# Optimization experiments

Measured on AMD Instinct MI355X. Metric: run time of the kernel, lower is better.

Reference implementation:

```python
import jax, jax.numpy as jnp
import numpy as np

B, S, D, H = 2, 2048, 1024, 16
HD = D // H  # head_dim = 64


def setup_inputs() -> dict:
    key = jax.random.key(0)
    ks = jax.random.split(key, 9)
    sc = 1.0 / np.sqrt(D)
    return {
        "X": jax.random.normal(ks[0], (B, S, D), jnp.float32),
        "Wq": jax.random.normal(ks[1], (D, D), jnp.float32) * sc,
        "bq": jnp.zeros((D,), jnp.float32),
        "Wk": jax.random.normal(ks[2], (D, D), jnp.float32) * sc,
        "bk": jnp.zeros((D,), jnp.float32),
        "Wv": jax.random.normal(ks[3], (D, D), jnp.float32) * sc,
        "bv": jnp.zeros((D,), jnp.float32),
        "Wo": jax.random.normal(ks[4], (D, D), jnp.float32) * sc,
        "bo": jnp.zeros((D,), jnp.float32),
    }


def reference(X, Wq, bq, Wk, bk, Wv, bv, Wo, bo):
    b, s, d = X.shape
    q = (X @ Wq + bq).reshape(b, s, H, HD).transpose(0, 2, 1, 3)  # [B,H,S,HD]
    k = (X @ Wk + bk).reshape(b, s, H, HD).transpose(0, 2, 1, 3)
    v = (X @ Wv + bv).reshape(b, s, H, HD).transpose(0, 2, 1, 3)
    score = jnp.einsum("bhqd,bhkd->bhqk", q, k) / jnp.sqrt(jnp.float32(HD))
    causal = jnp.tril(jnp.ones((s, s), bool))  # [S,S]
    score = jnp.where(causal[None, None], score, -jnp.inf)
    attn = jax.nn.softmax(score, axis=-1)
    out = jnp.einsum("bhqk,bhkd->bhqd", attn, v)  # [B,H,S,HD]
    out = out.transpose(0, 2, 1, 3).reshape(b, s, d)
    return out @ Wo + bo
```

## Files before the change

kernel.cpp:

```cpp
#include <hip/hip_runtime.h>
#include <hip/hip_bf16.h>
#include <math.h>

#define B_SZ 2
#define S_SZ 2048
#define D_SZ 1024
#define H_SZ 16
#define HD_SZ 64
constexpr int M_ROWS = B_SZ * S_SZ;

typedef __bf16 bf16x8 __attribute__((ext_vector_type(8)));
typedef __bf16 bf16x4 __attribute__((ext_vector_type(4)));
typedef float f32x4 __attribute__((ext_vector_type(4)));

#define GLOAD_LDS16(gsrc, ldst)                                              \
  __builtin_amdgcn_global_load_lds(                                          \
      (const __attribute__((address_space(1))) void*)(gsrc),                 \
      (__attribute__((address_space(3))) void*)(ldst), 16, 0, 0)

__global__ __launch_bounds__(256) void cvt_bf16(const float* __restrict__ in,
                                                __bf16* __restrict__ out,
                                                int n8) {
  const int i = blockIdx.x * 256 + threadIdx.x;
  if (i >= n8) return;
  const float4 a = *reinterpret_cast<const float4*>(&in[i * 8]);
  const float4 b = *reinterpret_cast<const float4*>(&in[i * 8 + 4]);
  bf16x8 o;
  o[0] = (__bf16)a.x; o[1] = (__bf16)a.y; o[2] = (__bf16)a.z; o[3] = (__bf16)a.w;
  o[4] = (__bf16)b.x; o[5] = (__bf16)b.y; o[6] = (__bf16)b.z; o[7] = (__bf16)b.w;
  *reinterpret_cast<bf16x8*>(&out[i * 8]) = o;
}

__global__ __launch_bounds__(256) void cvt_w_t_all(const float* __restrict__ W0,
                                                   const float* __restrict__ W1,
                                                   const float* __restrict__ W2,
                                                   const float* __restrict__ W3,
                                                   __bf16* __restrict__ Wt) {
  __shared__ float Ts[32][33];
  const int z = blockIdx.z;
  const float* W = z == 0 ? W0 : (z == 1 ? W1 : (z == 2 ? W2 : W3));
  __bf16* out = Wt + (size_t)z * 1024 * 1024;
  const int k0 = blockIdx.x * 32, n0 = blockIdx.y * 32;
  const int tr = threadIdx.x >> 3;
  const int tc = (threadIdx.x & 7) * 4;
  const float4 v = *reinterpret_cast<const float4*>(&W[(size_t)(k0 + tr) * 1024 + n0 + tc]);
  Ts[tr][tc + 0] = v.x;
  Ts[tr][tc + 1] = v.y;
  Ts[tr][tc + 2] = v.z;
  Ts[tr][tc + 3] = v.w;
  __syncthreads();
  bf16x4 o;
#pragma unroll
  for (int j = 0; j < 4; ++j) o[j] = (__bf16)Ts[tc + j][tr];
  *reinterpret_cast<bf16x4*>(&out[(size_t)(n0 + tr) * 1024 + k0 + tc]) = o;
}

__global__ __launch_bounds__(256) void transpose_v(const __bf16* __restrict__ V,
                                                   __bf16* __restrict__ Vt) {
  constexpr int TST = 66;
  __shared__ __bf16 T[64 * TST];
  const int bh = blockIdx.y;
  const int s0 = blockIdx.x * 64;
  const size_t base = (size_t)bh * S_SZ * HD_SZ;
  const int tid = threadIdx.x;
  for (int i = tid; i < 512; i += 256) {
    const int r = i >> 3, c = (i & 7) * 8;
    *reinterpret_cast<bf16x8*>(&T[r * TST + c]) =
        *reinterpret_cast<const bf16x8*>(&V[base + (size_t)(s0 + r) * 64 + c]);
  }
  __syncthreads();
  const size_t obase = (size_t)bh * HD_SZ * S_SZ;
  for (int i = tid; i < 512; i += 256) {
    const int d = i >> 3, c = (i & 7) * 8;
    bf16x8 o;
#pragma unroll
    for (int j = 0; j < 8; ++j) o[j] = T[(c + j) * TST + d];
    *reinterpret_cast<bf16x8*>(&Vt[obase + (size_t)d * S_SZ + s0 + c]) = o;
  }
}

template <int MODE, int BN>
__global__ __launch_bounds__(256) void gemm_mfma(
    const __bf16* __restrict__ Ab, const __bf16* __restrict__ Bt,
    const float* __restrict__ bias0, const float* __restrict__ bias1,
    const float* __restrict__ bias2, float* __restrict__ C0,
    __bf16* __restrict__ Q0, __bf16* __restrict__ K0, __bf16* __restrict__ V0,
    int M, int N, int K) {
  constexpr int NJ = BN / 32;
  __shared__ __bf16 As[2][128 * 32];
  __shared__ __bf16 Bs[2][BN * 32];
  __shared__ __bf16 Ep[(MODE == 1) ? 32 * 132 : 4];

  const int tid = threadIdx.x;
  const int lane = tid & 63;
  const int w = tid >> 6;
  const int lr = lane & 15, lg = lane >> 4;
  const int wr = w >> 1, wc = w & 1;
  const int bm = blockIdx.x * 128;
  const int bn = blockIdx.y * BN;

  const int r0 = tid >> 2, c0 = (tid & 3) * 8;
  const int r1 = (tid + 256) >> 2, c1 = ((tid + 256) & 3) * 8;
  const __bf16* aS0 = &Ab[(size_t)(bm + r0) * K + c0];
  const __bf16* aS1 = &Ab[(size_t)(bm + r1) * K + c1];
  const __bf16* bS0 = &Bt[(size_t)(bn + r0) * K + c0];
  const __bf16* bS1 = &Bt[(size_t)(bn + r1) * K + c1];

  f32x4 acc[4][NJ] = {};

  auto STAGE = [&](int buf) {
    GLOAD_LDS16(aS0, &As[buf][w * 512]);
    GLOAD_LDS16(aS1, &As[buf][2048 + w * 512]);
    GLOAD_LDS16(bS0, &Bs[buf][w * 512]);
    if constexpr (BN == 128) GLOAD_LDS16(bS1, &Bs[buf][2048 + w * 512]);
    aS0 += 32; aS1 += 32; bS0 += 32;
    if constexpr (BN == 128) bS1 += 32;
  };

  STAGE(0);
  asm volatile("s_waitcnt vmcnt(0)" ::: "memory");
  __builtin_amdgcn_s_barrier();
  __builtin_amdgcn_sched_barrier(0);
  int cur = 0;

  for (int k0 = 0; k0 < K; k0 += 32) {
    const bool has_next = (k0 + 32 < K);
    if (has_next) STAGE(cur ^ 1);
    if (k0) {
      if (has_next) {
        if constexpr (BN == 128)
          asm volatile("s_waitcnt vmcnt(4)" ::: "memory");
        else
          asm volatile("s_waitcnt vmcnt(3)" ::: "memory");
      } else {
        asm volatile("s_waitcnt vmcnt(0)" ::: "memory");
      }
      __builtin_amdgcn_s_barrier();
      __builtin_amdgcn_sched_barrier(0);
    }

    bf16x8 af[4], bfr[NJ];
#pragma unroll
    for (int i = 0; i < 4; ++i)
      af[i] = *reinterpret_cast<const bf16x8*>(&As[cur][(wr * 64 + i * 16 + lr) * 32 + lg * 8]);
#pragma unroll
    for (int j = 0; j < NJ; ++j)
      bfr[j] = *reinterpret_cast<const bf16x8*>(&Bs[cur][(wc * (BN / 2) + j * 16 + lr) * 32 + lg * 8]);
    __builtin_amdgcn_s_setprio(1);
#pragma unroll
    for (int i = 0; i < 4; ++i)
#pragma unroll
      for (int j = 0; j < NJ; ++j)
        acc[i][j] = __builtin_amdgcn_mfma_f32_16x16x32_bf16(af[i], bfr[j], acc[i][j], 0, 0, 0);
    __builtin_amdgcn_s_setprio(0);
    __builtin_amdgcn_sched_barrier(0);
    __builtin_amdgcn_s_barrier();
    cur ^= 1;
  }

  if (MODE == 0) {
#pragma unroll
    for (int j = 0; j < NJ; ++j) {
      const int n = bn + wc * (BN / 2) + j * 16 + lr;
      const float bs = bias0[n];
#pragma unroll
      for (int i = 0; i < 4; ++i) {
        const int mrow = bm + wr * 64 + i * 16 + lg * 4;
#pragma unroll
        for (int r = 0; r < 4; ++r)
          C0[(size_t)(mrow + r) * N + n] = acc[i][j][r] + bs;
      }
    }
  } else {
    const int which = bn >> 10;
    __bf16* dst = which == 0 ? Q0 : (which == 1 ? K0 : V0);
    const float* bp = which == 0 ? bias0 : (which == 1 ? bias1 : bias2);
    const float scale = which == 0 ? 0.18033688011112042f : 1.0f;
    float bias4[4];
#pragma unroll
    for (int j = 0; j < 4; ++j)
      bias4[j] = bp[(bn & 1023) + wc * 64 + j * 16 + lr];

#pragma unroll
    for (int i = 0; i < 4; ++i) {
      __syncthreads();
#pragma unroll
      for (int j = 0; j < 4; ++j) {
        const int colw = wc * 64 + j * 16 + lr;
#pragma unroll
        for (int r = 0; r < 4; ++r)
          Ep[(wr * 16 + lg * 4 + r) * 132 + colw] =
              (__bf16)((acc[i][j][r] + bias4[j]) * scale);
      }
      __syncthreads();
#pragma unroll
      for (int u = 0; u < 2; ++u) {
        const int c = tid + u * 256;
        const int er = c >> 4;
        const int off = (c & 15) * 8;
        const int m = bm + (er >> 4) * 64 + i * 16 + (er & 15);
        const int nn = (bn & 1023) + off;
        const int hh = nn >> 6, hd = nn & 63;
        const int bb = m >> 11, ss = m & (S_SZ - 1);
        *reinterpret_cast<bf16x8*>(
            &dst[(((size_t)(bb * H_SZ + hh)) * S_SZ + ss) * HD_SZ + hd]) =
            *reinterpret_cast<const bf16x8*>(&Ep[er * 132 + off]);
      }
    }
  }
}

__global__ __launch_bounds__(256) void attn_mfma(const __bf16* __restrict__ Q,
                                                 const __bf16* __restrict__ Kg,
                                                 const __bf16* __restrict__ Vtg,
                                                 __bf16* __restrict__ Aout) {
  constexpr int PST = 76;
  __shared__ __bf16 Ks[2][64 * 64];
  __shared__ __bf16 Vts[2][64 * 64];
  __shared__ __bf16 Ps[4][16 * PST];

  const int tid = threadIdx.x;
  const int lane = tid & 63;
  const int w = tid >> 6;
  const int lr = lane & 15;
  const int lg = lane >> 4;

  const int flat = blockIdx.x;
  const int g = flat >> 5;
  const int qb = (g < 16) ? (31 - g) : (g - 16);
  const int hb = flat & 31;
  const int h = hb >> 1, b = hb & 1;
  const size_t base = (size_t)(b * H_SZ + h) * S_SZ * HD_SZ;
  const int q0 = qb * 64 + w * 16;

  bf16x8 aq[2];
#pragma unroll
  for (int hh = 0; hh < 2; ++hh)
    aq[hh] = *reinterpret_cast<const bf16x8*>(
        &Q[base + (size_t)(q0 + lr) * 64 + hh * 32 + lg * 8]);

  const int srow = lane >> 3;
  const int schunk = (lane & 7) ^ srow;

  bf16x8 ones8;
#pragma unroll
  for (int j = 0; j < 8; ++j) ones8[j] = (__bf16)1.0f;

  f32x4 oacc[4] = {};
  f32x4 oacc_l = {};

  const int ntiles = qb + 1;

  const int rbA = w * 16, rbB = w * 16 + 8;
  const __bf16* kS0 = &Kg[base + (size_t)(rbA + srow) * 64 + schunk * 8];
  const __bf16* kS1 = &Kg[base + (size_t)(rbB + srow) * 64 + schunk * 8];
  const __bf16* vS0 = &Vtg[base + (size_t)(rbA + srow) * S_SZ + schunk * 8];
  const __bf16* vS1 = &Vtg[base + (size_t)(rbB + srow) * S_SZ + schunk * 8];

  auto ISSUE = [&](int buf) {
    GLOAD_LDS16(kS0, &Ks[buf][rbA * 64]);
    GLOAD_LDS16(kS1, &Ks[buf][rbB * 64]);
    GLOAD_LDS16(vS0, &Vts[buf][rbA * 64]);
    GLOAD_LDS16(vS1, &Vts[buf][rbB * 64]);
  };

  ISSUE(0);
  asm volatile("s_waitcnt vmcnt(0)" ::: "memory");
  __builtin_amdgcn_s_barrier();
  __builtin_amdgcn_sched_barrier(0);
  int cur = 0;

  for (int t0 = 0; t0 < ntiles; ++t0) {
    const bool has_next = (t0 + 1 < ntiles);
    if (has_next) {
      kS0 += 64 * 64; kS1 += 64 * 64;
      vS0 += 64;      vS1 += 64;
      ISSUE(cur ^ 1);
    }
    if (t0) {
      if (has_next)
        asm volatile("s_waitcnt vmcnt(4)" ::: "memory");
      else
        asm volatile("s_waitcnt vmcnt(0)" ::: "memory");
      __builtin_amdgcn_s_barrier();
      __builtin_amdgcn_sched_barrier(0);
    }

    f32x4 s[4];
    __builtin_amdgcn_s_setprio(1);
#pragma unroll
    for (int t = 0; t < 4; ++t) {
      const int row = t * 16 + lr;
      const bf16x8 k0f = *reinterpret_cast<const bf16x8*>(
          &Ks[cur][row * 64 + ((lg ^ (lr & 7)) * 8)]);
      const bf16x8 k1f = *reinterpret_cast<const bf16x8*>(
          &Ks[cur][row * 64 + (((4 | lg) ^ (lr & 7)) * 8)]);
      f32x4 z = (f32x4){0.f, 0.f, 0.f, 0.f};
      z = __builtin_amdgcn_mfma_f32_16x16x32_bf16(aq[0], k0f, z, 0, 0, 0);
      z = __builtin_amdgcn_mfma_f32_16x16x32_bf16(aq[1], k1f, z, 0, 0, 0);
      s[t] = z;
    }
    __builtin_amdgcn_s_setprio(0);

    if (t0 == qb) {
#pragma unroll
      for (int t = 0; t < 4; ++t) {
        const int key = t0 * 64 + t * 16 + lr;
#pragma unroll
        for (int r = 0; r < 4; ++r) {
          const int qrow = q0 + lg * 4 + r;
          if (key > qrow) s[t][r] = -INFINITY;
        }
      }
    }

#pragma unroll
    for (int t = 0; t < 4; ++t)
#pragma unroll
      for (int r = 0; r < 4; ++r)
        Ps[w][(lg * 4 + r) * PST + t * 16 + lr] =
            (__bf16)__builtin_amdgcn_exp2f(s[t][r]);
    asm volatile("s_waitcnt lgkmcnt(0)" ::: "memory");
    __builtin_amdgcn_sched_barrier(0);

    __builtin_amdgcn_s_setprio(1);
#pragma unroll
    for (int kh = 0; kh < 2; ++kh) {
      const bf16x8 pa = *reinterpret_cast<const bf16x8*>(
          &Ps[w][lr * PST + kh * 32 + lg * 8]);
#pragma unroll
      for (int dc = 0; dc < 4; ++dc) {
        const int row = dc * 16 + lr;
        const bf16x8 vf = *reinterpret_cast<const bf16x8*>(
            &Vts[cur][row * 64 + (((kh * 4 + lg) ^ (lr & 7)) * 8)]);
        oacc[dc] = __builtin_amdgcn_mfma_f32_16x16x32_bf16(pa, vf, oacc[dc], 0, 0, 0);
      }
      oacc_l = __builtin_amdgcn_mfma_f32_16x16x32_bf16(pa, ones8, oacc_l, 0, 0, 0);
    }
    __builtin_amdgcn_s_setprio(0);

    __builtin_amdgcn_sched_barrier(0);
    __builtin_amdgcn_s_barrier();
    cur ^= 1;
  }

#pragma unroll
  for (int r = 0; r < 4; ++r) {
    const float inv = 1.f / oacc_l[r];
#pragma unroll
    for (int dc = 0; dc < 4; ++dc)
      Ps[w][(lg * 4 + r) * PST + dc * 16 + lr] = (__bf16)(oacc[dc][r] * inv);
  }
  asm volatile("s_waitcnt lgkmcnt(0)" ::: "memory");
  __builtin_amdgcn_sched_barrier(0);
#pragma unroll
  for (int u = 0; u < 2; ++u) {
    const int c = lane + u * 64;
    const int row = c >> 3;
    const int off = (c & 7) * 8;
    const int qg = q0 + row;
    *reinterpret_cast<bf16x8*>(
        &Aout[(size_t)(b * S_SZ + qg) * D_SZ + h * 64 + off]) =
        *reinterpret_cast<const bf16x8*>(&Ps[w][row * PST + off]);
  }
}

extern "C" void kernel_launch(void* const* d_in, const int* in_sizes, int n_in,
                              void* d_out, int out_size, void* d_ws,
                              size_t ws_size, hipStream_t stream) {
  const float* X = (const float*)d_in[0];
  const float* Wq = (const float*)d_in[1];
  const float* bq = (const float*)d_in[2];
  const float* Wk = (const float*)d_in[3];
  const float* bk = (const float*)d_in[4];
  const float* Wv = (const float*)d_in[5];
  const float* bv = (const float*)d_in[6];
  const float* Wo = (const float*)d_in[7];
  const float* bo = (const float*)d_in[8];
  float* out = (float*)d_out;

  const size_t elems = (size_t)M_ROWS * D_SZ;
  const size_t welems = (size_t)D_SZ * D_SZ;
  __bf16* Xb = (__bf16*)d_ws;
  __bf16* Wt = Xb + elems;
  __bf16* Q = Wt + 4 * welems;
  __bf16* K = Q + elems;
  __bf16* V = K + elems;
  __bf16* Vt = V + elems;
  __bf16* Ahb = Vt + elems;

  cvt_bf16<<<(int)(elems / 8 / 256), 256, 0, stream>>>(X, Xb, (int)(elems / 8));
  cvt_w_t_all<<<dim3(32, 32, 4), 256, 0, stream>>>(Wq, Wk, Wv, Wo, Wt);

  gemm_mfma<1, 128><<<dim3(M_ROWS / 128, 3072 / 128), 256, 0, stream>>>(
      Xb, Wt, bq, bk, bv, nullptr, Q, K, V, M_ROWS, 3072, D_SZ);

  transpose_v<<<dim3(32, 32), 256, 0, stream>>>(V, Vt);

  attn_mfma<<<dim3(1024), 256, 0, stream>>>(Q, K, Vt, Ahb);

  gemm_mfma<0, 64><<<dim3(M_ROWS / 128, D_SZ / 64), 256, 0, stream>>>(
      Ahb, Wt + 3 * welems, bo, nullptr, nullptr, out, nullptr, nullptr,
      nullptr, M_ROWS, D_SZ, D_SZ);
}
```

Measured before the change: 110.5 us.

## Fuse input conversion kernels and restage V loads in attention

Merges the X-to-bf16 conversion and the weight transpose/convert kernels into one launch, with a fifth grid slice handling X. This removes one kernel launch. In attention, V drops from double-buffered to single-buffered: its load is issued at the top of each tile and waited on just before the PV MFMAs, while K stays double-buffered. Query-block scheduling is also reordered into interleaved groups of eight to balance causal work. Together these cut LDS use and may raise occupancy, at the cost of less latency hiding for V and an extra barrier per tile.

```diff
diff --git a/kernel.cpp b/kernel.cpp
--- a/kernel.cpp
+++ b/kernel.cpp
@@ -18,41 +18,45 @@
       (const __attribute__((address_space(1))) void*)(gsrc),                 \
       (__attribute__((address_space(3))) void*)(ldst), 16, 0, 0)
 
-__global__ __launch_bounds__(256) void cvt_bf16(const float* __restrict__ in,
-                                                __bf16* __restrict__ out,
-                                                int n8) {
-  const int i = blockIdx.x * 256 + threadIdx.x;
-  if (i >= n8) return;
-  const float4 a = *reinterpret_cast<const float4*>(&in[i * 8]);
-  const float4 b = *reinterpret_cast<const float4*>(&in[i * 8 + 4]);
-  bf16x8 o;
-  o[0] = (__bf16)a.x; o[1] = (__bf16)a.y; o[2] = (__bf16)a.z; o[3] = (__bf16)a.w;
-  o[4] = (__bf16)b.x; o[5] = (__bf16)b.y; o[6] = (__bf16)b.z; o[7] = (__bf16)b.w;
-  *reinterpret_cast<bf16x8*>(&out[i * 8]) = o;
-}
-
-__global__ __launch_bounds__(256) void cvt_w_t_all(const float* __restrict__ W0,
-                                                   const float* __restrict__ W1,
-                                                   const float* __restrict__ W2,
-                                                   const float* __restrict__ W3,
-                                                   __bf16* __restrict__ Wt) {
+__global__ __launch_bounds__(256) void prep_all(const float* __restrict__ X,
+                                                const float* __restrict__ W0,
+                                                const float* __restrict__ W1,
+                                                const float* __restrict__ W2,
+                                                const float* __restrict__ W3,
+                                                __bf16* __restrict__ Xb,
+                                                __bf16* __restrict__ Wt) {
   __shared__ float Ts[32][33];
   const int z = blockIdx.z;
-  const float* W = z == 0 ? W0 : (z == 1 ? W1 : (z == 2 ? W2 : W3));
-  __bf16* out = Wt + (size_t)z * 1024 * 1024;
-  const int k0 = blockIdx.x * 32, n0 = blockIdx.y * 32;
-  const int tr = threadIdx.x >> 3;
-  const int tc = (threadIdx.x & 7) * 4;
-  const float4 v = *reinterpret_cast<const float4*>(&W[(size_t)(k0 + tr) * 1024 + n0 + tc]);
-  Ts[tr][tc + 0] = v.x;
-  Ts[tr][tc + 1] = v.y;
-  Ts[tr][tc + 2] = v.z;
-  Ts[tr][tc + 3] = v.w;
-  __syncthreads();
-  bf16x4 o;
-#pragma unroll
-  for (int j = 0; j < 4; ++j) o[j] = (__bf16)Ts[tc + j][tr];
-  *reinterpret_cast<bf16x4*>(&out[(size_t)(n0 + tr) * 1024 + k0 + tc]) = o;
+  if (z < 4) {
+    const float* W = z == 0 ? W0 : (z == 1 ? W1 : (z == 2 ? W2 : W3));
+    __bf16* out = Wt + (size_t)z * 1024 * 1024;
+    const int k0 = blockIdx.x * 32, n0 = blockIdx.y * 32;
+    const int tr = threadIdx.x >> 3;
+    const int tc = (threadIdx.x & 7) * 4;
+    const float4 v =
+        *reinterpret_cast<const float4*>(&W[(size_t)(k0 + tr) * 1024 + n0 + tc]);
+    Ts[tr][tc + 0] = v.x;
+    Ts[tr][tc + 1] = v.y;
+    Ts[tr][tc + 2] = v.z;
+    Ts[tr][tc + 3] = v.w;
+    __syncthreads();
+    bf16x4 o;
+#pragma unroll
+    for (int j = 0; j < 4; ++j) o[j] = (__bf16)Ts[tc + j][tr];
+    *reinterpret_cast<bf16x4*>(&out[(size_t)(n0 + tr) * 1024 + k0 + tc]) = o;
+  } else {
+    const int flat = blockIdx.y * 32 + blockIdx.x;
+    const size_t e0 = ((size_t)flat * 256 + threadIdx.x) * 16;
+#pragma unroll
+    for (int half = 0; half < 2; ++half) {
+      const float4 a = *reinterpret_cast<const float4*>(&X[e0 + half * 8]);
+      const float4 b = *reinterpret_cast<const float4*>(&X[e0 + half * 8 + 4]);
+      bf16x8 o;
+      o[0] = (__bf16)a.x; o[1] = (__bf16)a.y; o[2] = (__bf16)a.z; o[3] = (__bf16)a.w;
+      o[4] = (__bf16)b.x; o[5] = (__bf16)b.y; o[6] = (__bf16)b.z; o[7] = (__bf16)b.w;
+      *reinterpret_cast<bf16x8*>(&Xb[e0 + half * 8]) = o;
+    }
+  }
 }
 
 __global__ __launch_bounds__(256) void transpose_v(const __bf16* __restrict__ V,
@@ -216,7 +220,7 @@
                                                  __bf16* __restrict__ Aout) {
   constexpr int PST = 76;
   __shared__ __bf16 Ks[2][64 * 64];
-  __shared__ __bf16 Vts[2][64 * 64];
+  __shared__ __bf16 Vts[64 * 64];
   __shared__ __bf16 Ps[4][16 * PST];
 
   const int tid = threadIdx.x;
@@ -227,7 +231,9 @@
 
   const int flat = blockIdx.x;
   const int g = flat >> 5;
-  const int qb = (g < 16) ? (31 - g) : (g - 16);
+  const int r8 = g & 7, j4 = g >> 3;
+  const int qb = (j4 == 0) ? r8 : (j4 == 1) ? (15 - r8)
+                                : (j4 == 2) ? (16 + r8) : (31 - r8);
   const int hb = flat & 31;
   const int h = hb >> 1, b = hb & 1;
   const size_t base = (size_t)(b * H_SZ + h) * S_SZ * HD_SZ;
@@ -257,33 +263,23 @@
   const __bf16* vS0 = &Vtg[base + (size_t)(rbA + srow) * S_SZ + schunk * 8];
   const __bf16* vS1 = &Vtg[base + (size_t)(rbB + srow) * S_SZ + schunk * 8];
 
-  auto ISSUE = [&](int buf) {
-    GLOAD_LDS16(kS0, &Ks[buf][rbA * 64]);
-    GLOAD_LDS16(kS1, &Ks[buf][rbB * 64]);
-    GLOAD_LDS16(vS0, &Vts[buf][rbA * 64]);
-    GLOAD_LDS16(vS1, &Vts[buf][rbB * 64]);
-  };
-
-  ISSUE(0);
-  asm volatile("s_waitcnt vmcnt(0)" ::: "memory");
-  __builtin_amdgcn_s_barrier();
-  __builtin_amdgcn_sched_barrier(0);
+  GLOAD_LDS16(kS0, &Ks[0][rbA * 64]);
+  GLOAD_LDS16(kS1, &Ks[0][rbB * 64]);
   int cur = 0;
 
   for (int t0 = 0; t0 < ntiles; ++t0) {
+    asm volatile("s_waitcnt vmcnt(0)" ::: "memory");
+    __builtin_amdgcn_s_barrier();
+    __builtin_amdgcn_sched_barrier(0);
+
+    GLOAD_LDS16(vS0, &Vts[rbA * 64]);
+    GLOAD_LDS16(vS1, &Vts[rbB * 64]);
+    vS0 += 64; vS1 += 64;
     const bool has_next = (t0 + 1 < ntiles);
     if (has_next) {
       kS0 += 64 * 64; kS1 += 64 * 64;
-      vS0 += 64;      vS1 += 64;
-      ISSUE(cur ^ 1);
-    }
-    if (t0) {
-      if (has_next)
-        asm volatile("s_waitcnt vmcnt(4)" ::: "memory");
-      else
-        asm volatile("s_waitcnt vmcnt(0)" ::: "memory");
-      __builtin_amdgcn_s_barrier();
-      __builtin_amdgcn_sched_barrier(0);
+      GLOAD_LDS16(kS0, &Ks[cur ^ 1][rbA * 64]);
+      GLOAD_LDS16(kS1, &Ks[cur ^ 1][rbB * 64]);
     }
 
     f32x4 s[4];
@@ -323,6 +319,13 @@
     asm volatile("s_waitcnt lgkmcnt(0)" ::: "memory");
     __builtin_amdgcn_sched_barrier(0);
 
+    if (has_next)
+      asm volatile("s_waitcnt vmcnt(2)" ::: "memory");
+    else
+      asm volatile("s_waitcnt vmcnt(0)" ::: "memory");
+    __builtin_amdgcn_s_barrier();
+    __builtin_amdgcn_sched_barrier(0);
+
     __builtin_amdgcn_s_setprio(1);
 #pragma unroll
     for (int kh = 0; kh < 2; ++kh) {
@@ -332,15 +335,13 @@
       for (int dc = 0; dc < 4; ++dc) {
         const int row = dc * 16 + lr;
         const bf16x8 vf = *reinterpret_cast<const bf16x8*>(
-            &Vts[cur][row * 64 + (((kh * 4 + lg) ^ (lr & 7)) * 8)]);
+            &Vts[row * 64 + (((kh * 4 + lg) ^ (lr & 7)) * 8)]);
         oacc[dc] = __builtin_amdgcn_mfma_f32_16x16x32_bf16(pa, vf, oacc[dc], 0, 0, 0);
       }
       oacc_l = __builtin_amdgcn_mfma_f32_16x16x32_bf16(pa, ones8, oacc_l, 0, 0, 0);
     }
     __builtin_amdgcn_s_setprio(0);
-
     __builtin_amdgcn_sched_barrier(0);
-    __builtin_amdgcn_s_barrier();
     cur ^= 1;
   }
 
@@ -389,8 +390,7 @@
   __bf16* Vt = V + elems;
   __bf16* Ahb = Vt + elems;
 
-  cvt_bf16<<<(int)(elems / 8 / 256), 256, 0, stream>>>(X, Xb, (int)(elems / 8));
-  cvt_w_t_all<<<dim3(32, 32, 4), 256, 0, stream>>>(Wq, Wk, Wv, Wo, Wt);
+  prep_all<<<dim3(32, 32, 5), 256, 0, stream>>>(X, Wq, Wk, Wv, Wo, Xb, Wt);
 
   gemm_mfma<1, 128><<<dim3(M_ROWS / 128, 3072 / 128), 256, 0, stream>>>(
       Xb, Wt, bq, bk, bv, nullptr, Q, K, V, M_ROWS, 3072, D_SZ);
```

New measurement: 112.8 us. 1.02x slower.
